# Kernel tuning notes

Measured on AMD Instinct MI355X. Metric: run time of the kernel, lower is better.

Reference implementation:

```python
import jax, jax.numpy as jnp
import numpy as np

N = 50000
E = 800000
IN_FEATS = 256
N_HIDDEN = 64
N_CLASSES = 40
HEADS = (4, 1)
NEG_SLOPE = 0.2  # DGL GATConv default


def gat_layer(x, src, dst, W, attn_l, attn_r, bias, n_heads, out_dim, activation):
    """One dglnn.GATConv layer (eval mode: dropout disabled).

    x: [N, F_in]; src/dst: [E] edge endpoints; W: [F_in, H*D];
    attn_l/attn_r: [H, D]; bias: [H*D]. Returns [N, H, D].
    """
    n = x.shape[0]
    z = (x @ W).reshape(n, n_heads, out_dim)            # [N, H, D]
    el = jnp.sum(z * attn_l[None], axis=-1)            # [N, H]
    er = jnp.sum(z * attn_r[None], axis=-1)            # [N, H]
    e = jax.nn.leaky_relu(el[src] + er[dst], NEG_SLOPE)  # [E, H]
    # segment softmax over incoming edges of each dst node
    m = jax.ops.segment_max(e, dst, num_segments=n)     # [N, H]
    a = jnp.exp(e - m[dst])                             # [E, H]
    s = jax.ops.segment_sum(a, dst, num_segments=n)     # [N, H]
    alpha = a / s[dst]                                  # [E, H]
    msg = alpha[:, :, None] * z[src]                    # [E, H, D]
    out = jax.ops.segment_sum(msg, dst, num_segments=n)  # [N, H, D]
    out = out + bias.reshape(1, n_heads, out_dim)
    if activation is not None:
        out = activation(out)
    return out


def setup_inputs() -> dict:
    key = jax.random.key(0)
    ks = jax.random.split(key, 12)
    H0, H1 = HEADS
    d_in1 = N_HIDDEN * H0
    def glorot(k, shape):
        fan = sum(shape[:2]) if len(shape) > 1 else shape[0]
        return jax.random.normal(k, shape, jnp.float32) * (2.0 / fan) ** 0.5
    return {
        "x": jax.random.normal(ks[0], (N, IN_FEATS), jnp.float32),
        "src": jax.random.randint(ks[1], (E,), 0, N),
        "dst": jax.random.randint(ks[2], (E,), 0, N),
        "W0": glorot(ks[3], (IN_FEATS, H0 * N_HIDDEN)),
        "attn_l0": glorot(ks[4], (H0, N_HIDDEN)),
        "attn_r0": glorot(ks[5], (H0, N_HIDDEN)),
        "bias0": jnp.zeros((H0 * N_HIDDEN,), jnp.float32),
        "W1": glorot(ks[6], (d_in1, H1 * N_CLASSES)),
        "attn_l1": glorot(ks[7], (H1, N_CLASSES)),
        "attn_r1": glorot(ks[8], (H1, N_CLASSES)),
        "bias1": jnp.zeros((H1 * N_CLASSES,), jnp.float32),
    }


def reference(x, src, dst, W0, attn_l0, attn_r0, bias0, W1, attn_l1, attn_r1, bias1):
    H0, H1 = HEADS
    # layer 0: GATConv + ELU, then flatten heads (l==0 branch)
    h = gat_layer(x, src, dst, W0, attn_l0, attn_r0, bias0,
                  H0, N_HIDDEN, jax.nn.elu)              # [N, H0, D]
    h = h.reshape(h.shape[0], -1)                        # [N, H0*D]
    # layer 1 (last): GATConv, no activation, head-mean (l==1 branch)
    h = gat_layer(h, src, dst, W1, attn_l1, attn_r1, bias1,
                  H1, N_CLASSES, None)                   # [N, H1, C]
    return h.mean(axis=1)                                # [N, C]
```

## Files before the change

kernel.cpp:

```cpp
#include <hip/hip_runtime.h>
#include <math.h>

using bf16x8 = __attribute__((ext_vector_type(8))) short;
using f32x4  = __attribute__((ext_vector_type(4))) float;

__device__ __forceinline__ unsigned short f2bf(float v) {
  unsigned int b = __float_as_uint(v);
  unsigned int r = (b + 0x7fffu + ((b >> 16) & 1u)) >> 16;
  return (unsigned short)r;
}
__device__ __forceinline__ float bf2f(unsigned short u) {
  return __uint_as_float(((unsigned int)u) << 16);
}


__global__ void mega0_kernel(const float* __restrict__ W0f, unsigned short* __restrict__ Bp0,
                             const float* __restrict__ W1f, unsigned short* __restrict__ Bp1,
                             const int* __restrict__ dst, int* __restrict__ deg,
                             int* __restrict__ slot, int E) {
  int bx = blockIdx.x;
  if (bx >= 38) {
    int t = (bx - 38) * 256 + threadIdx.x;
    if (t < E) slot[t] = atomicAdd(&deg[dst[t]], 1);
    return;
  }
  int idx = bx * 256 + threadIdx.x;
  if (idx < 8192) {
    int lane = idx & 63, s = (idx >> 6) & 7, t = idx >> 9;
    int n = t * 16 + (lane & 15), quad = lane >> 4;
    unsigned short* o = Bp0 + (size_t)idx * 8;
    #pragma unroll
    for (int j = 0; j < 8; ++j) {
      int k = s * 32 + quad * 8 + j;
      o[j] = f2bf(W0f[(size_t)k * 256 + n]);
    }
  } else if (idx < 8192 + 1536) {
    int i1 = idx - 8192;
    int lane = i1 & 63, s = (i1 >> 6) & 7, t = i1 >> 9;
    int n = t * 16 + (lane & 15), quad = lane >> 4;
    unsigned short* o = Bp1 + (size_t)i1 * 8;
    #pragma unroll
    for (int j = 0; j < 8; ++j) {
      int k = s * 32 + quad * 8 + j;
      o[j] = (n < 40) ? f2bf(W1f[(size_t)k * 40 + n]) : 0;
    }
  }
}


__global__ void block_sum_kernel(const int* __restrict__ deg, int* __restrict__ bsum, int n) {
  __shared__ int red[4];
  int t = threadIdx.x, i = blockIdx.x * 256 + t;
  int v = (i < n) ? deg[i] : 0;
  #pragma unroll
  for (int off = 32; off; off >>= 1) v += __shfl_xor(v, off);
  if ((t & 63) == 0) red[t >> 6] = v;
  __syncthreads();
  if (t == 0) bsum[blockIdx.x] = red[0] + red[1] + red[2] + red[3];
}

__global__ void scan_bsum_kernel(const int* __restrict__ bsum, int* __restrict__ boffs,
                                 int* __restrict__ offsets, int nb, int n) {
  __shared__ int tmp[1024];
  int t = threadIdx.x;
  int v = (t < nb) ? bsum[t] : 0;
  tmp[t] = v;
  __syncthreads();
  #pragma unroll
  for (int off = 1; off < 1024; off <<= 1) {
    int add = (t >= off) ? tmp[t - off] : 0;
    __syncthreads();
    tmp[t] += add;
    __syncthreads();
  }
  if (t < nb) boffs[t] = tmp[t] - v;
  if (t == 1023) offsets[n] = tmp[1023];
}

__global__ void write_offsets_kernel(const int* __restrict__ deg, const int* __restrict__ boffs,
                                     int* __restrict__ offsets, int n) {
  __shared__ int tmp[256];
  int t = threadIdx.x, i = blockIdx.x * 256 + t;
  int v = (i < n) ? deg[i] : 0;
  tmp[t] = v;
  __syncthreads();
  #pragma unroll
  for (int off = 1; off < 256; off <<= 1) {
    int add = (t >= off) ? tmp[t - off] : 0;
    __syncthreads();
    tmp[t] += add;
    __syncthreads();
  }
  if (i < n) offsets[i] = boffs[blockIdx.x] + tmp[t] - v;
}


__global__ __launch_bounds__(512) void mega2_kernel(
    const float* __restrict__ A, const unsigned short* __restrict__ Bp,
    unsigned short* __restrict__ Zb,
    const float* __restrict__ al, const float* __restrict__ arr,
    float* __restrict__ el, float* __restrict__ er, int M,
    const int* __restrict__ src, const int* __restrict__ dst,
    const int* __restrict__ offs, const int* __restrict__ slot,
    int* __restrict__ ssrc, int E, int nG, int nC) {
  int bx = blockIdx.x;
  int tid = threadIdx.x;

  if (bx >= nG) {
    int stride = nC * 512;
    for (int e = (bx - nG) * 512 + tid; e < E; e += stride) {
      int p = offs[dst[e]] + slot[e];
      ssrc[p] = src[e];
    }
    return;
  }

  int gx = bx >> 1, y = bx & 1;
  int wid = tid >> 6, lane = tid & 63;
  int quad = lane >> 4, col16 = lane & 15;
  int wr = wid >> 1, wc = wid & 1;
  int rowbase = gx * 256 + wr * 64;

  const float* aptr[4];
  #pragma unroll
  for (int rt = 0; rt < 4; ++rt) {
    int m = rowbase + rt * 16 + col16;
    if (m > M - 1) m = M - 1;
    aptr[rt] = A + (size_t)m * 256 + quad * 8;
  }

  f32x4 acc[4][4];
  #pragma unroll
  for (int rt = 0; rt < 4; ++rt)
    #pragma unroll
    for (int ct = 0; ct < 4; ++ct) acc[rt][ct] = {0.f, 0.f, 0.f, 0.f};

  const bf16x8* BpV = (const bf16x8*)Bp;

  auto loadA = [&](bf16x8* fr, int s) {
    #pragma unroll
    for (int rt = 0; rt < 4; ++rt) {
      const float* ap = aptr[rt] + s * 32;
      float4 a0 = *(const float4*)ap;
      float4 a1 = *(const float4*)(ap + 4);
      fr[rt][0] = (short)f2bf(a0.x); fr[rt][1] = (short)f2bf(a0.y);
      fr[rt][2] = (short)f2bf(a0.z); fr[rt][3] = (short)f2bf(a0.w);
      fr[rt][4] = (short)f2bf(a1.x); fr[rt][5] = (short)f2bf(a1.y);
      fr[rt][6] = (short)f2bf(a1.z); fr[rt][7] = (short)f2bf(a1.w);
    }
  };

  bf16x8 afc[4];
  loadA(afc, 0);
  for (int s = 0; s < 8; ++s) {
    bf16x8 afn[4];
    if (s < 7) loadA(afn, s + 1);
    #pragma unroll
    for (int ct = 0; ct < 4; ++ct) {
      bf16x8 bf = BpV[y * 4096 + ((wc * 4 + ct) * 8 + s) * 64 + lane];
      #pragma unroll
      for (int rt = 0; rt < 4; ++rt)
        acc[rt][ct] = __builtin_amdgcn_mfma_f32_16x16x32_bf16(afc[rt], bf, acc[rt][ct], 0, 0, 0);
    }
    if (s < 7) {
      #pragma unroll
      for (int rt = 0; rt < 4; ++rt) afc[rt] = afn[rt];
    }
  }

  int hw = y * 2 + wc;
  float al_c[4], ar_c[4];
  #pragma unroll
  for (int ct = 0; ct < 4; ++ct) {
    int col = y * 128 + (wc * 4 + ct) * 16 + col16;
    al_c[ct] = al[col];
    ar_c[ct] = arr[col];
  }

  #pragma unroll
  for (int rt = 0; rt < 4; ++rt) {
    int row0 = rowbase + rt * 16 + quad * 4;
    #pragma unroll
    for (int r = 0; r < 4; ++r) {
      int row = row0 + r;
      if (row < M) {
        #pragma unroll
        for (int ct = 0; ct < 4; ++ct) {
          int col = y * 128 + (wc * 4 + ct) * 16 + col16;
          Zb[(size_t)row * 256 + col] = f2bf(acc[rt][ct][r]);
        }
      }
      float pe = 0.f, pr = 0.f;
      #pragma unroll
      for (int ct = 0; ct < 4; ++ct) {
        float zv = acc[rt][ct][r];
        pe += zv * al_c[ct];
        pr += zv * ar_c[ct];
      }
      pe += __shfl_xor(pe, 1); pr += __shfl_xor(pr, 1);
      pe += __shfl_xor(pe, 2); pr += __shfl_xor(pr, 2);
      pe += __shfl_xor(pe, 4); pr += __shfl_xor(pr, 4);
      pe += __shfl_xor(pe, 8); pr += __shfl_xor(pr, 8);
      if (col16 == 0 && row < M) {
        el[(size_t)row * 4 + hw] = pe;
        er[(size_t)row * 4 + hw] = pr;
      }
    }
  }
}


__global__ __launch_bounds__(256) void gemm1_mfma_kernel(
    const unsigned short* __restrict__ Ab, const unsigned short* __restrict__ Bp,
    unsigned short* __restrict__ Zb,
    const float* __restrict__ al, const float* __restrict__ arr,
    float* __restrict__ el, float* __restrict__ er, int M) {
  int wid = threadIdx.x >> 6, lane = threadIdx.x & 63;
  int quad = lane >> 4, col16 = lane & 15;
  int m = blockIdx.x * 64 + wid * 16 + col16;

  f32x4 acc[3];
  #pragma unroll
  for (int t = 0; t < 3; ++t) acc[t] = {0.f, 0.f, 0.f, 0.f};

  const bf16x8* BpV = (const bf16x8*)Bp;

  for (int s = 0; s < 8; ++s) {
    bf16x8 af;
    if (m < M) {
      af = *(const bf16x8*)(Ab + (size_t)m * 256 + s * 32 + quad * 8);
    } else {
      #pragma unroll
      for (int j = 0; j < 8; ++j) af[j] = 0;
    }
    #pragma unroll
    for (int t = 0; t < 3; ++t) {
      bf16x8 bf = BpV[(t * 8 + s) * 64 + lane];
      acc[t] = __builtin_amdgcn_mfma_f32_16x16x32_bf16(af, bf, acc[t], 0, 0, 0);
    }
  }

  float al_c[3], ar_c[3];
  #pragma unroll
  for (int t = 0; t < 3; ++t) {
    int col = t * 16 + col16;
    al_c[t] = (col < 40) ? al[col] : 0.f;
    ar_c[t] = (col < 40) ? arr[col] : 0.f;
  }

  int row0 = blockIdx.x * 64 + wid * 16 + quad * 4;
  #pragma unroll
  for (int r = 0; r < 4; ++r) {
    int row = row0 + r;
    if (row < M) {
      #pragma unroll
      for (int t = 0; t < 3; ++t) {
        int col = t * 16 + col16;
        if (col < 40) Zb[(size_t)row * 40 + col] = f2bf(acc[t][r]);
      }
    }
    float pe = 0.f, pr = 0.f;
    #pragma unroll
    for (int t = 0; t < 3; ++t) {
      pe += acc[t][r] * al_c[t];
      pr += acc[t][r] * ar_c[t];
    }
    pe += __shfl_xor(pe, 1); pr += __shfl_xor(pr, 1);
    pe += __shfl_xor(pe, 2); pr += __shfl_xor(pr, 2);
    pe += __shfl_xor(pe, 4); pr += __shfl_xor(pr, 4);
    pe += __shfl_xor(pe, 8); pr += __shfl_xor(pr, 8);
    if (col16 == 0 && row < M) {
      el[row] = pe;
      er[row] = pr;
    }
  }
}


__global__ __launch_bounds__(256) void agg0_kernel(
    const int* __restrict__ offs, const int* __restrict__ ssrc,
    const float* __restrict__ el, const float* __restrict__ er,
    const unsigned short* __restrict__ zb, const float* __restrict__ bias,
    unsigned short* __restrict__ outb, int n) {
  __shared__ float sW[4][16][4];
  __shared__ int   sS[4][16];
  int wid  = threadIdx.x >> 6;
  int lane = threadIdx.x & 63;
  int node = blockIdx.x * 4 + wid;
  if (node >= n) return;
  int c = lane & 3, eoff = lane >> 2;
  int half = lane >> 5, colg = lane & 31, h2 = colg >> 3;
  int s0 = offs[node], s1 = offs[node + 1];
  float er_c = er[node * 4 + c];
  const unsigned short* zcol = zb + (colg << 3);

  float ssum = 0.f;
  float acc[8] = {0.f, 0.f, 0.f, 0.f, 0.f, 0.f, 0.f, 0.f};
  for (int base = s0; base < s1; base += 16) {
    int cnt = min(16, s1 - base);
    if (eoff < cnt) {
      int esrc = ssrc[base + eoff];
      float v = el[esrc * 4 + c] + er_c;
      v = v > 0.f ? v : 0.2f * v;
      sW[wid][eoff][c] = expf(v);
      if (c == 0) sS[wid][eoff] = esrc;
    }
    for (int j = 0; j < cnt; j += 8) {
      float w[4];
      bf16x8 zu[4];
      #pragma unroll
      for (int u = 0; u < 4; ++u) {
        int jj = j + 2 * u + half;
        if (jj < cnt) {
          w[u] = sW[wid][jj][h2];
          int sn = sS[wid][jj];
          zu[u] = *(const bf16x8*)(zcol + (size_t)sn * 256);
        } else {
          w[u] = 0.f;
          #pragma unroll
          for (int i = 0; i < 8; ++i) zu[u][i] = 0;
        }
      }
      #pragma unroll
      for (int u = 0; u < 4; ++u) {
        ssum += w[u];
        #pragma unroll
        for (int i = 0; i < 8; ++i)
          acc[i] += w[u] * bf2f((unsigned short)zu[u][i]);
      }
    }
  }

  ssum += __shfl_xor(ssum, 32);
  #pragma unroll
  for (int i = 0; i < 8; ++i) acc[i] += __shfl_xor(acc[i], 32);

  float inv = (s1 > s0) ? 1.f / ssum : 0.f;
  if (half == 0) {
    const float4 b0v = *(const float4*)(bias + (colg << 3));
    const float4 b1v = *(const float4*)(bias + (colg << 3) + 4);
    float bb[8] = {b0v.x, b0v.y, b0v.z, b0v.w, b1v.x, b1v.y, b1v.z, b1v.w};
    bf16x8 u;
    #pragma unroll
    for (int i = 0; i < 8; ++i) {
      float o = acc[i] * inv + bb[i];
      o = o > 0.f ? o : expm1f(o);
      u[i] = (short)f2bf(o);
    }
    *(bf16x8*)(outb + (size_t)node * 256 + (colg << 3)) = u;
  }
}


__global__ __launch_bounds__(256) void agg1_kernel(
    const int* __restrict__ offs, const int* __restrict__ ssrc,
    const float* __restrict__ el, const float* __restrict__ er,
    const unsigned short* __restrict__ zb, const float* __restrict__ bias,
    float* __restrict__ out, int n) {
  __shared__ float sW[4][64];
  __shared__ int   sS[4][64];
  int wid  = threadIdx.x >> 6;
  int lane = threadIdx.x & 63;
  int node = blockIdx.x * 4 + wid;
  if (node >= n) return;
  int half = lane >> 5, d = lane & 31;
  int s0 = offs[node], s1 = offs[node + 1];
  float ern = er[node];

  float ssum = 0.f;
  float2 acc = make_float2(0.f, 0.f);
  for (int base = s0; base < s1; base += 64) {
    int cnt = min(64, s1 - base);
    if (lane < cnt) {
      int esrc = ssrc[base + lane];
      float v = el[esrc] + ern;
      v = v > 0.f ? v : 0.2f * v;
      sW[wid][lane] = expf(v);
      sS[wid][lane] = esrc;
    }
    for (int j = 0; j < cnt; j += 2) {
      int jj = j + half;
      float w = (jj < cnt) ? sW[wid][jj] : 0.f;
      int sn = sS[wid][(jj < cnt) ? jj : (cnt - 1)];
      ssum += w;
      if (d < 20) {
        unsigned zp = *(const unsigned*)(zb + (size_t)sn * 40 + (d << 1));
        acc.x += w * bf2f((unsigned short)(zp & 0xffffu));
        acc.y += w * bf2f((unsigned short)(zp >> 16));
      }
    }
  }

  ssum  += __shfl_xor(ssum, 32);
  acc.x += __shfl_xor(acc.x, 32);
  acc.y += __shfl_xor(acc.y, 32);

  float inv = (s1 > s0) ? 1.f / ssum : 0.f;
  if (half == 0 && d < 20) {
    float2 o;
    o.x = acc.x * inv + bias[(d << 1) + 0];
    o.y = acc.y * inv + bias[(d << 1) + 1];
    *(float2*)(out + (size_t)node * 40 + (d << 1)) = o;
  }
}


extern "C" void kernel_launch(void* const* d_in, const int* in_sizes, int n_in,
                              void* d_out, int out_size, void* d_ws, size_t ws_size,
                              hipStream_t stream) {
  const float* x   = (const float*)d_in[0];
  const int*   src = (const int*)d_in[1];
  const int*   dst = (const int*)d_in[2];
  const float* W0  = (const float*)d_in[3];
  const float* al0 = (const float*)d_in[4];
  const float* ar0 = (const float*)d_in[5];
  const float* b0  = (const float*)d_in[6];
  const float* W1  = (const float*)d_in[7];
  const float* al1 = (const float*)d_in[8];
  const float* ar1 = (const float*)d_in[9];
  const float* b1  = (const float*)d_in[10];
  float* out = (float*)d_out;

  const int N = in_sizes[0] / 256;
  const int E = in_sizes[1];
  const int NB = (N + 255) / 256;

  char* ws = (char*)d_ws;
  size_t off = 0;
  auto alloc = [&](size_t bytes) {
    void* p = ws + off;
    off = (off + bytes + 255) & ~(size_t)255;
    return p;
  };
  unsigned short* z0b = (unsigned short*)alloc((size_t)N * 256 * 2);
  unsigned short* h0b = (unsigned short*)alloc((size_t)N * 256 * 2);
  unsigned short* z1b = (unsigned short*)alloc((size_t)N * 40 * 2);
  unsigned short* w0p = (unsigned short*)alloc((size_t)16 * 8 * 64 * 8 * 2);
  unsigned short* w1p = (unsigned short*)alloc((size_t)3 * 8 * 64 * 8 * 2);
  float* el0  = (float*)alloc((size_t)N * 4 * 4);
  float* er0  = (float*)alloc((size_t)N * 4 * 4);
  float* el1  = (float*)alloc((size_t)N * 4);
  float* er1  = (float*)alloc((size_t)N * 4);
  int* deg    = (int*)alloc((size_t)N * 4);
  int* offs   = (int*)alloc((size_t)(N + 1) * 4);
  int* slot   = (int*)alloc((size_t)E * 4);
  int* bsum   = (int*)alloc((size_t)NB * 4);
  int* boffs  = (int*)alloc((size_t)NB * 4);
  int* ssrc   = (int*)alloc((size_t)E * 4);
  (void)off; (void)ws_size; (void)n_in; (void)out_size;

  const int nG = ((N + 255) / 256) * 2;
  const int nH = (E + 255) / 256;
  const int nC = 391;

  hipMemsetAsync(deg, 0, (size_t)N * 4, stream);
  mega0_kernel<<<38 + nH, 256, 0, stream>>>(W0, w0p, W1, w1p, dst, deg, slot, E);
  block_sum_kernel<<<NB, 256, 0, stream>>>(deg, bsum, N);
  scan_bsum_kernel<<<1, 1024, 0, stream>>>(bsum, boffs, offs, NB, N);
  write_offsets_kernel<<<NB, 256, 0, stream>>>(deg, boffs, offs, N);
  mega2_kernel<<<nG + nC, 512, 0, stream>>>(x, w0p, z0b, al0, ar0, el0, er0, N,
                                            src, dst, offs, slot, ssrc, E, nG, nC);
  agg0_kernel<<<(N + 3) / 4, 256, 0, stream>>>(offs, ssrc, el0, er0, z0b, b0, h0b, N);
  gemm1_mfma_kernel<<<(N + 63) / 64, 256, 0, stream>>>(h0b, w1p, z1b, al1, ar1, el1, er1, N);
  agg1_kernel<<<(N + 3) / 4, 256, 0, stream>>>(offs, ssrc, el1, er1, z1b, b1, out, N);
}
```

Baseline: 306.7 us.

## Overlap degree histogram with layer-0 GEMM instead of CSR scatter

Moves the atomic degree-count/slot pass out of the weight-pack kernel and fuses it into the layer-0 GEMM launch as extra blocks, so the histogram overlaps the GEMM. The CSR scatter of source indices, previously piggybacked on the GEMM launch, becomes its own kernel after the offset scan. The weight pack now runs alone as a small kernel. The aim is to hide the atomic histogram behind GEMM work, at the cost of one more launch and leaving the CSR scatter serialized.

```diff
diff --git a/kernel.cpp b/kernel.cpp
--- a/kernel.cpp
+++ b/kernel.cpp
@@ -14,17 +14,9 @@
 }
 
 
-__global__ void mega0_kernel(const float* __restrict__ W0f, unsigned short* __restrict__ Bp0,
-                             const float* __restrict__ W1f, unsigned short* __restrict__ Bp1,
-                             const int* __restrict__ dst, int* __restrict__ deg,
-                             int* __restrict__ slot, int E) {
-  int bx = blockIdx.x;
-  if (bx >= 38) {
-    int t = (bx - 38) * 256 + threadIdx.x;
-    if (t < E) slot[t] = atomicAdd(&deg[dst[t]], 1);
-    return;
-  }
-  int idx = bx * 256 + threadIdx.x;
+__global__ void pack_kernel(const float* __restrict__ W0f, unsigned short* __restrict__ Bp0,
+                            const float* __restrict__ W1f, unsigned short* __restrict__ Bp1) {
+  int idx = blockIdx.x * 256 + threadIdx.x;
   if (idx < 8192) {
     int lane = idx & 63, s = (idx >> 6) & 7, t = idx >> 9;
     int n = t * 16 + (lane & 15), quad = lane >> 4;
@@ -95,23 +87,19 @@
 }
 
 
-__global__ __launch_bounds__(512) void mega2_kernel(
+__global__ __launch_bounds__(512) void mega_hg_kernel(
     const float* __restrict__ A, const unsigned short* __restrict__ Bp,
     unsigned short* __restrict__ Zb,
     const float* __restrict__ al, const float* __restrict__ arr,
     float* __restrict__ el, float* __restrict__ er, int M,
-    const int* __restrict__ src, const int* __restrict__ dst,
-    const int* __restrict__ offs, const int* __restrict__ slot,
-    int* __restrict__ ssrc, int E, int nG, int nC) {
+    const int* __restrict__ dst, int* __restrict__ deg, int* __restrict__ slot,
+    int E, int nG) {
   int bx = blockIdx.x;
   int tid = threadIdx.x;
 
   if (bx >= nG) {
-    int stride = nC * 512;
-    for (int e = (bx - nG) * 512 + tid; e < E; e += stride) {
-      int p = offs[dst[e]] + slot[e];
-      ssrc[p] = src[e];
-    }
+    int t = (bx - nG) * 512 + tid;
+    if (t < E) slot[t] = atomicAdd(&deg[dst[t]], 1);
     return;
   }
 
@@ -206,6 +194,18 @@
         er[(size_t)row * 4 + hw] = pr;
       }
     }
+  }
+}
+
+
+__global__ __launch_bounds__(256) void csr_kernel(
+    const int* __restrict__ src, const int* __restrict__ dst,
+    const int* __restrict__ offs, const int* __restrict__ slot,
+    int* __restrict__ ssrc, int E) {
+  int e = blockIdx.x * 256 + threadIdx.x;
+  if (e < E) {
+    int p = offs[dst[e]] + slot[e];
+    ssrc[p] = src[e];
   }
 }
 
@@ -450,16 +450,17 @@
   (void)off; (void)ws_size; (void)n_in; (void)out_size;
 
   const int nG = ((N + 255) / 256) * 2;
-  const int nH = (E + 255) / 256;
-  const int nC = 391;
+  const int nH512 = (E + 511) / 512;
+  const int nCSR = (E + 255) / 256;
 
   hipMemsetAsync(deg, 0, (size_t)N * 4, stream);
-  mega0_kernel<<<38 + nH, 256, 0, stream>>>(W0, w0p, W1, w1p, dst, deg, slot, E);
+  pack_kernel<<<38, 256, 0, stream>>>(W0, w0p, W1, w1p);
+  mega_hg_kernel<<<nG + nH512, 512, 0, stream>>>(x, w0p, z0b, al0, ar0, el0, er0, N,
+                                                 dst, deg, slot, E, nG);
   block_sum_kernel<<<NB, 256, 0, stream>>>(deg, bsum, N);
   scan_bsum_kernel<<<1, 1024, 0, stream>>>(bsum, boffs, offs, NB, N);
   write_offsets_kernel<<<NB, 256, 0, stream>>>(deg, boffs, offs, N);
-  mega2_kernel<<<nG + nC, 512, 0, stream>>>(x, w0p, z0b, al0, ar0, el0, er0, N,
-                                            src, dst, offs, slot, ssrc, E, nG, nC);
+  csr_kernel<<<nCSR, 256, 0, stream>>>(src, dst, offs, slot, ssrc, E);
   agg0_kernel<<<(N + 3) / 4, 256, 0, stream>>>(offs, ssrc, el0, er0, z0b, b0, h0b, N);
   gemm1_mfma_kernel<<<(N + 63) / 64, 256, 0, stream>>>(h0b, w1p, z1b, al1, ar1, el1, er1, N);
   agg1_kernel<<<(N + 3) / 4, 256, 0, stream>>>(offs, ssrc, el1, er1, z1b, b1, out, N);
```

Result: no change. 302.5 us (-1.4%).
